# Kernel tuning notes

Hardware: AMD Instinct MI355X
Metric: run time of the kernel (lower is better)

Reference implementation:

```python
import jax, jax.numpy as jnp
import numpy as np

D_MODEL = 1024
NUM_HEADS = 16
DILATION_RATES = [2, 2, 2]
SEGMENT_SIZES = [64, 128, 256]
BATCH = 2
SEQ_LEN = 8192
N_LAYERS = len(SEGMENT_SIZES)


def setup_inputs() -> dict:
    key = jax.random.key(0)
    ks = jax.random.split(key, 5)
    d = D_MODEL
    scale = 1.0 / np.sqrt(d)
    x = jax.random.normal(ks[0], (BATCH, SEQ_LEN, d), dtype=jnp.float32)
    # Per-layer fused QKV + output projection params (stacked over layers)
    Wqkv = jax.random.normal(ks[1], (N_LAYERS, d, 3 * d), dtype=jnp.float32) * scale
    bqkv = jnp.zeros((N_LAYERS, 3 * d), dtype=jnp.float32)
    Wo = jax.random.normal(ks[2], (N_LAYERS, d, d), dtype=jnp.float32) * scale
    bo = jnp.zeros((N_LAYERS, d), dtype=jnp.float32)
    return {"x": x, "Wqkv": Wqkv, "bqkv": bqkv, "Wo": Wo, "bo": bo}


def _dilated_attention(x, Wqkv, bqkv, Wo, bo, seg, dr):
    # x: [B, S, D]. Segment, then dilate-stride within each segment.
    B, S, D = x.shape
    H = NUM_HEADS
    hd = D // H
    x4 = x.reshape(B, S // seg, seg, D)[:, :, ::dr, :]  # [B, N, s, D], s = seg//dr
    s = seg // dr
    N = S // seg
    qkv = jnp.einsum('bnsd,de->bnse', x4, Wqkv) + bqkv  # [B, N, s, 3D]
    q, k, v = jnp.split(qkv, 3, axis=-1)
    q = q.reshape(B, N, s, H, hd)
    k = k.reshape(B, N, s, H, hd)
    v = v.reshape(B, N, s, H, hd)
    # attention within each dilated segment
    scores = jnp.einsum('bnqhd,bnkhd->bnhqk', q, k) * (1.0 / np.sqrt(hd))
    attn = jax.nn.softmax(scores, axis=-1)
    o = jnp.einsum('bnhqk,bnkhd->bnqhd', attn, v).reshape(B, N, s, D)
    o = jnp.einsum('bnsd,de->bnse', o, Wo) + bo
    return o.reshape(B, N * s, D)  # [B, S/dr, D]


def reference(x, Wqkv, bqkv, Wo, bo):
    outs = []
    for i in range(N_LAYERS):
        outs.append(_dilated_attention(x, Wqkv[i], bqkv[i], Wo[i], bo[i],
                                       SEGMENT_SIZES[i], DILATION_RATES[i]))
    return jnp.stack(outs, axis=0).sum(axis=0)
```

## Files before the change

kernel.cpp:

```cpp
#include <hip/hip_runtime.h>
#include <hip/hip_bf16.h>
#include <stdint.h>

typedef unsigned short u16;
typedef short bf16x8 __attribute__((ext_vector_type(8)));
typedef u16   u16x8  __attribute__((ext_vector_type(8)));
typedef u16   u16x4  __attribute__((ext_vector_type(4)));
typedef float f32x4  __attribute__((ext_vector_type(4)));

__device__ inline u16 f2bf(float f) {
    uint32_t u = __builtin_bit_cast(uint32_t, f);
    uint32_t r = (u + 0x7FFFu + ((u >> 16) & 1u)) >> 16;
    return (u16)r;
}

__device__ inline void gload16(const void* g, void* l) {
    __builtin_amdgcn_global_load_lds((const __attribute__((address_space(1))) void*)g,
                                     (__attribute__((address_space(3))) void*)l, 16, 0, 0);
}

#define MFMA16(a, b, c) __builtin_amdgcn_mfma_f32_16x16x32_bf16((a), (b), (c), 0, 0, 0)

__global__ __launch_bounds__(256) void k_prep_xe(const float* __restrict__ x,
                                                 u16* __restrict__ xe) {
    int row = blockIdx.x;
    int b = row >> 12, tt = row & 4095;
    const float* src = x + ((size_t)b * 8192 + 2 * (size_t)tt) * 1024;
    float4 v = ((const float4*)src)[threadIdx.x];
    u16x4 o = { f2bf(v.x), f2bf(v.y), f2bf(v.z), f2bf(v.w) };
    *(u16x4*)(xe + (size_t)row * 1024 + threadIdx.x * 4) = o;
}

__global__ __launch_bounds__(256) void k_transpose_cast(
    const float* __restrict__ src, u16* __restrict__ dst,
    int srcCols, size_t srcLayerStride, int dstStride, int dstRowPer, int dstColPer) {
    int k0 = blockIdx.x * 64, e0 = blockIdx.y * 64, layer = blockIdx.z;
    const float* s = src + (size_t)layer * srcLayerStride;
    __shared__ u16 T[64][66];
    int t = threadIdx.x;
#pragma unroll
    for (int p = 0; p < 16; ++p) {
        int l = p * 256 + t;
        int kl = l >> 6, el = l & 63;
        T[kl][el] = f2bf(s[(size_t)(k0 + kl) * srcCols + e0 + el]);
    }
    __syncthreads();
    int rowBase = layer * dstRowPer + e0;
    int colBase = layer * dstColPer + k0;
#pragma unroll
    for (int p = 0; p < 16; ++p) {
        int l = p * 256 + t;
        int eo = l >> 6, ko = l & 63;
        dst[(size_t)(rowBase + eo) * dstStride + colBase + ko] = T[ko][eo];
    }
}

template <bool BF16OUT>
__global__ __launch_bounds__(256) void k_gemm_bt(
    const u16* __restrict__ A, const u16* __restrict__ B, void* __restrict__ C,
    const float* __restrict__ bias0, const float* __restrict__ bias1,
    const float* __restrict__ bias2, int K, int lda, int ldb, int ldc) {
    __shared__ __align__(16) char smem[16384];
    const int tid = threadIdx.x;
    const int lane = tid & 63, wave = tid >> 6;
    const int wr = wave >> 1, wc = wave & 1;
    const int row0 = blockIdx.x * 128, col0 = blockIdx.y * 128;
    f32x4 acc[4][4] = {};
    const int nk = K >> 5;
    const char* Abase = (const char*)(A + (size_t)row0 * lda);
    const char* Bbase = (const char*)(B + (size_t)col0 * ldb);
    char* ldsA = smem;
    char* ldsB = smem + 8192;
    const size_t lda2 = (size_t)lda * 2, ldb2 = (size_t)ldb * 2;
    const int c0 = tid;
    const int c1 = tid + 256;

    for (int ks = 0; ks < nk; ++ks) {
        const size_t kb0 = (size_t)(ks * 32) * 2;
        gload16(Abase + (size_t)(c0 >> 2) * lda2 + kb0 + (c0 & 3) * 16, ldsA + wave * 1024);
        gload16(Abase + (size_t)(c1 >> 2) * lda2 + kb0 + (c1 & 3) * 16, ldsA + 4096 + wave * 1024);
        gload16(Bbase + (size_t)(c0 >> 2) * ldb2 + kb0 + (c0 & 3) * 16, ldsB + wave * 1024);
        gload16(Bbase + (size_t)(c1 >> 2) * ldb2 + kb0 + (c1 & 3) * 16, ldsB + 4096 + wave * 1024);
        __syncthreads();
        bf16x8 af[4], bfr[4];
        const int kb = (lane >> 4) << 4;
#pragma unroll
        for (int mt = 0; mt < 4; ++mt)
            af[mt] = *(const bf16x8*)(ldsA + (wr * 64 + mt * 16 + (lane & 15)) * 64 + kb);
#pragma unroll
        for (int nt = 0; nt < 4; ++nt)
            bfr[nt] = *(const bf16x8*)(ldsB + (wc * 64 + nt * 16 + (lane & 15)) * 64 + kb);
#pragma unroll
        for (int mt = 0; mt < 4; ++mt)
#pragma unroll
            for (int nt = 0; nt < 4; ++nt)
                acc[mt][nt] = MFMA16(af[mt], bfr[nt], acc[mt][nt]);
        __syncthreads();
    }
    const int g = lane >> 4, cl = lane & 15;
#pragma unroll
    for (int nt = 0; nt < 4; ++nt) {
        int col = col0 + wc * 64 + nt * 16 + cl;
        float bs = bias0[col];
        if (bias1) bs += bias1[col];
        if (bias2) bs += bias2[col];
#pragma unroll
        for (int mt = 0; mt < 4; ++mt) {
#pragma unroll
            for (int r = 0; r < 4; ++r) {
                int row = row0 + wr * 64 + mt * 16 + g * 4 + r;
                float v = acc[mt][nt][r] + bs;
                if (BF16OUT)
                    ((u16*)C)[(size_t)row * ldc + col] = f2bf(v);
                else
                    ((float*)C)[(size_t)row * ldc + col] = v;
            }
        }
    }
}

template <int S>
__global__ __launch_bounds__(256) void k_attn(const u16* __restrict__ qkv,
                                              u16* __restrict__ ab, int layer) {
    constexpr int NCT = S / 16;
    constexpr int RPW = (S == 32) ? 1 : S / 64;
    constexpr int ACTIVE = (S == 32) ? 2 : 4;
    constexpr int KST = S / 32;
    constexpr int VSTRIDE = 2 * S;
    constexpr int VMASK = VSTRIDE / 16 - 1;

    __shared__ __align__(16) char KS[S * 128];
    __shared__ __align__(16) char VTS[64 * VSTRIDE];
    __shared__ __align__(16) char PS[S * VSTRIDE];

    const int per_b = (4096 / S) * 16;
    const int b = blockIdx.x / per_b;
    const int r0 = blockIdx.x % per_b;
    const int n = r0 >> 4, h = r0 & 15;
    const int token0 = b * 4096 + n * S;
    const int colQ = layer * 3072 + h * 64;
    const int tid = threadIdx.x, lane = tid & 63, wave = tid >> 6;

    constexpr int CHUNKS = S / 32;
#pragma unroll
    for (int c = 0; c < CHUNKS; ++c) {
        int lc = c * 256 + tid;
        int row = lc >> 3, off = (lc & 7) * 16;
        const char* base = (const char*)qkv + ((size_t)(token0 + row) * 9216 + colQ) * 2 + off;
        u16x8 kv = *(const u16x8*)(base + 1024 * 2);
        *(u16x8*)(KS + row * 128 + (off ^ ((row & 7) << 4))) = kv;
        u16x8 vv = *(const u16x8*)(base + 2048 * 2);
        int cb = off >> 1;
#pragma unroll
        for (int e = 0; e < 8; ++e) {
            int col = cb + e;
            *(u16*)(VTS + col * VSTRIDE + ((row * 2) ^ ((col & VMASK) << 4))) = vv[e];
        }
    }
    __syncthreads();

    f32x4 sacc[RPW][NCT] = {};
    if (wave < ACTIVE) {
#pragma unroll
        for (int rl = 0; rl < RPW; ++rl) {
            int rt = wave * RPW + rl;
#pragma unroll
            for (int ks2 = 0; ks2 < 2; ++ks2) {
                int qrow = token0 + rt * 16 + (lane & 15);
                int kbyte = ks2 * 64 + ((lane >> 4) << 4);
                bf16x8 aq = *(const bf16x8*)((const char*)qkv +
                              ((size_t)qrow * 9216 + colQ) * 2 + kbyte);
#pragma unroll
                for (int ct = 0; ct < NCT; ++ct) {
                    int krow = ct * 16 + (lane & 15);
                    bf16x8 bk = *(const bf16x8*)(KS + krow * 128 + (kbyte ^ ((krow & 7) << 4)));
                    sacc[rl][ct] = MFMA16(aq, bk, sacc[rl][ct]);
                }
            }
        }
#pragma unroll
        for (int rl = 0; rl < RPW; ++rl) {
            int rt = wave * RPW + rl;
#pragma unroll
            for (int r = 0; r < 4; ++r) {
                float vals[NCT];
                float m = -1e30f;
#pragma unroll
                for (int ct = 0; ct < NCT; ++ct) {
                    vals[ct] = sacc[rl][ct][r] * 0.125f;
                    m = fmaxf(m, vals[ct]);
                }
#pragma unroll
                for (int d = 1; d < 16; d <<= 1) m = fmaxf(m, __shfl_xor(m, d, 64));
                float sum = 0.f;
#pragma unroll
                for (int ct = 0; ct < NCT; ++ct) {
                    float p = exp2f((vals[ct] - m) * 1.44269504f);
                    vals[ct] = p;
                    sum += p;
                }
#pragma unroll
                for (int d = 1; d < 16; d <<= 1) sum += __shfl_xor(sum, d, 64);
                float inv = 1.0f / sum;
                int row = rt * 16 + ((lane >> 4) << 2) + r;
#pragma unroll
                for (int ct = 0; ct < NCT; ++ct) {
                    int col = ct * 16 + (lane & 15);
                    *(u16*)(PS + row * VSTRIDE + ((col * 2) ^ ((row & VMASK) << 4))) =
                        f2bf(vals[ct] * inv);
                }
            }
        }
    }
    __syncthreads();

    if (wave < ACTIVE) {
        const int colA = layer * 1024 + h * 64;
#pragma unroll
        for (int rl = 0; rl < RPW; ++rl) {
            int rt = wave * RPW + rl;
            f32x4 oacc[4] = {};
#pragma unroll
            for (int ks2 = 0; ks2 < KST; ++ks2) {
                int kbyte = ks2 * 64 + ((lane >> 4) << 4);
                int prow = rt * 16 + (lane & 15);
                bf16x8 ap = *(const bf16x8*)(PS + prow * VSTRIDE + (kbyte ^ ((prow & VMASK) << 4)));
#pragma unroll
                for (int ct = 0; ct < 4; ++ct) {
                    int vcol = ct * 16 + (lane & 15);
                    bf16x8 bv = *(const bf16x8*)(VTS + vcol * VSTRIDE + (kbyte ^ ((vcol & VMASK) << 4)));
                    oacc[ct] = MFMA16(ap, bv, oacc[ct]);
                }
            }
#pragma unroll
            for (int ct = 0; ct < 4; ++ct) {
#pragma unroll
                for (int r = 0; r < 4; ++r) {
                    int row = token0 + rt * 16 + ((lane >> 4) << 2) + r;
                    int col = colA + ct * 16 + (lane & 15);
                    ab[(size_t)row * 3072 + col] = f2bf(oacc[ct][r]);
                }
            }
        }
    }
}

extern "C" void kernel_launch(void* const* d_in, const int* in_sizes, int n_in,
                              void* d_out, int out_size, void* d_ws, size_t ws_size,
                              hipStream_t stream) {
    const float* x    = (const float*)d_in[0];
    const float* Wqkv = (const float*)d_in[1];
    const float* bqkv = (const float*)d_in[2];
    const float* Wo   = (const float*)d_in[3];
    const float* bo   = (const float*)d_in[4];

    char* ws = (char*)d_ws;
    u16* XE    = (u16*)(ws);
    u16* WQKVT = (u16*)(ws + 16777216);
    u16* WOT   = (u16*)(ws + 35651584);
    u16* QKVB  = (u16*)(ws + 41943040);
    u16* ABUF  = (u16*)(ws + 192937984);

    k_prep_xe<<<8192, 256, 0, stream>>>(x, XE);
    k_transpose_cast<<<dim3(16, 48, 3), 256, 0, stream>>>(
        Wqkv, WQKVT, 3072, (size_t)1024 * 3072, 1024, 3072, 0);
    k_transpose_cast<<<dim3(16, 16, 3), 256, 0, stream>>>(
        Wo, WOT, 1024, (size_t)1024 * 1024, 3072, 0, 1024);

    k_gemm_bt<true><<<dim3(64, 72), 256, 0, stream>>>(
        XE, WQKVT, QKVB, bqkv, nullptr, nullptr, 1024, 1024, 1024, 9216);

    k_attn<32><<<4096, 256, 0, stream>>>(QKVB, ABUF, 0);
    k_attn<64><<<2048, 256, 0, stream>>>(QKVB, ABUF, 1);
    k_attn<128><<<1024, 256, 0, stream>>>(QKVB, ABUF, 2);

    k_gemm_bt<false><<<dim3(64, 8), 256, 0, stream>>>(
        ABUF, WOT, d_out, bo, bo + 1024, bo + 2048, 3072, 3072, 3072, 1024);
}
```

Measured before the change: 366.5 us.

## Replace QKV GEMM with 256x256 tile, 4-stage pipelined, swizzled kernel

Adds a new 512-thread GEMM kernel with 256x256 output tiles, a 4-deep LDS ring filled by direct global-to-LDS loads, XOR-swizzled LDS layout, and explicit barriers with scheduling priority to overlap loads with MFMA work. Workgroups are remapped in groups of eight for L2 locality. It replaces the 128x128 GEMM for the QKV projection (8192x9216x1024). The aim is more data reuse per tile and hidden memory latency. The cost is 128KB of LDS per block, which limits occupancy, and a more fragile pipeline schedule.

```diff
diff --git a/kernel.cpp b/kernel.cpp
--- a/kernel.cpp
+++ b/kernel.cpp
@@ -17,6 +17,12 @@
 __device__ inline void gload16(const void* g, void* l) {
     __builtin_amdgcn_global_load_lds((const __attribute__((address_space(1))) void*)g,
                                      (__attribute__((address_space(3))) void*)l, 16, 0, 0);
+}
+
+__device__ inline void pin_barrier() {
+    __builtin_amdgcn_sched_barrier(0);
+    __builtin_amdgcn_s_barrier();
+    __builtin_amdgcn_sched_barrier(0);
 }
 
 #define MFMA16(a, b, c) __builtin_amdgcn_mfma_f32_16x16x32_bf16((a), (b), (c), 0, 0, 0)
@@ -53,6 +59,114 @@
         int eo = l >> 6, ko = l & 63;
         dst[(size_t)(rowBase + eo) * dstStride + colBase + ko] = T[ko][eo];
     }
+}
+
+__global__ __launch_bounds__(512, 2) void k_gemm256(
+    const u16* __restrict__ A, const u16* __restrict__ B, u16* __restrict__ C,
+    const float* __restrict__ bias, int K, int lda, int ldb, int ldc,
+    int gxmask, int gxshift) {
+    __shared__ __align__(16) char smem[131072];
+    const int tid = threadIdx.x;
+    const int lane = tid & 63, wave = tid >> 6;
+    const int wr = wave >> 2, wc = wave & 3;
+
+    const int nwg = gridDim.x;
+    const int bid = blockIdx.x;
+    const int cpx = nwg >> 3;
+    const int swz = (bid & 7) * cpx + (bid >> 3);
+    const int bx = swz & gxmask;
+    const int by = swz >> gxshift;
+    const int row0 = bx << 8, col0 = by << 8;
+
+#define SA(q) (smem + (q) * 32768)
+#define SB(q) (smem + (q) * 32768 + 16384)
+
+    const int c0 = tid, c1 = tid + 512;
+    const int rA0 = ((c0 >> 6) << 4) + ((c0 >> 2) & 15);
+    const int rA1 = ((c1 >> 6) << 4) + ((c1 >> 2) & 15);
+    const int cb0 = ((c0 & 3) * 16) ^ (((c0 >> 5) & 1) << 5);
+    const int cb1 = ((c1 & 3) * 16) ^ (((c1 >> 5) & 1) << 5);
+    const size_t lda2 = (size_t)lda * 2, ldb2 = (size_t)ldb * 2;
+    const char* pA0 = (const char*)A + (size_t)(row0 + rA0) * lda2 + cb0;
+    const char* pA1 = (const char*)A + (size_t)(row0 + rA1) * lda2 + cb1;
+    const char* pB0 = (const char*)B + (size_t)(col0 + rA0) * ldb2 + cb0;
+    const char* pB1 = (const char*)B + (size_t)(col0 + rA1) * ldb2 + cb1;
+    const int ldsOff0 = wave * 1024, ldsOff1 = 8192 + wave * 1024;
+
+#define STAGE_A(q, kof) do { gload16(pA0 + (kof), SA(q) + ldsOff0); \
+                             gload16(pA1 + (kof), SA(q) + ldsOff1); } while (0)
+#define STAGE_B(q, kof) do { gload16(pB0 + (kof), SB(q) + ldsOff0); \
+                             gload16(pB1 + (kof), SB(q) + ldsOff1); } while (0)
+
+    const int lane_off = (lane & 15) * 64 + (((lane >> 4) << 4) ^ (((lane >> 3) & 1) << 5));
+
+    f32x4 acc[8][4] = {};
+    const int nt = K >> 5;
+
+    STAGE_A(0, 0);   STAGE_B(0, 0);
+    STAGE_A(1, 64);  STAGE_B(1, 64);
+    STAGE_A(2, 128); STAGE_B(2, 128);
+    __builtin_amdgcn_sched_barrier(0);
+    asm volatile("s_waitcnt vmcnt(8)" ::: "memory");
+    pin_barrier();
+
+    for (int t = 0; t < nt; ++t) {
+        const int q = t & 3, q3 = (t + 3) & 3;
+        const int ts = (t + 3 < nt) ? (t + 3) : (nt - 1);
+        const size_t kof = (size_t)ts * 64;
+        const char* aRd = SA(q) + wr * 8192 + lane_off;
+        const char* bRd = SB(q) + wc * 4096 + lane_off;
+
+        bf16x8 af[4], bg[4];
+#pragma unroll
+        for (int i = 0; i < 4; ++i) af[i] = *(const bf16x8*)(aRd + i * 1024);
+#pragma unroll
+        for (int i = 0; i < 4; ++i) bg[i] = *(const bf16x8*)(bRd + i * 1024);
+        STAGE_A(q3, kof);
+        pin_barrier();
+        __builtin_amdgcn_s_setprio(1);
+#pragma unroll
+        for (int m = 0; m < 4; ++m)
+#pragma unroll
+            for (int n = 0; n < 4; ++n)
+                acc[m][n] = MFMA16(af[m], bg[n], acc[m][n]);
+        __builtin_amdgcn_s_setprio(0);
+        pin_barrier();
+
+#pragma unroll
+        for (int i = 0; i < 4; ++i) af[i] = *(const bf16x8*)(aRd + (4 + i) * 1024);
+        STAGE_B(q3, kof);
+        __builtin_amdgcn_sched_barrier(0);
+        asm volatile("s_waitcnt vmcnt(8)" ::: "memory");
+        pin_barrier();
+        __builtin_amdgcn_s_setprio(1);
+#pragma unroll
+        for (int m = 0; m < 4; ++m)
+#pragma unroll
+            for (int n = 0; n < 4; ++n)
+                acc[4 + m][n] = MFMA16(af[m], bg[n], acc[4 + m][n]);
+        __builtin_amdgcn_s_setprio(0);
+        pin_barrier();
+    }
+
+    const int g4 = (lane >> 4) << 2, cl = lane & 15;
+#pragma unroll
+    for (int n = 0; n < 4; ++n) {
+        int col = col0 + wc * 64 + n * 16 + cl;
+        float bs = bias[col];
+#pragma unroll
+        for (int m = 0; m < 8; ++m) {
+#pragma unroll
+            for (int r = 0; r < 4; ++r) {
+                int row = row0 + wr * 128 + m * 16 + g4 + r;
+                C[(size_t)row * ldc + col] = f2bf(acc[m][n][r] + bs);
+            }
+        }
+    }
+#undef SA
+#undef SB
+#undef STAGE_A
+#undef STAGE_B
 }
 
 template <bool BF16OUT>
@@ -267,8 +381,8 @@
     k_transpose_cast<<<dim3(16, 16, 3), 256, 0, stream>>>(
         Wo, WOT, 1024, (size_t)1024 * 1024, 3072, 0, 1024);
 
-    k_gemm_bt<true><<<dim3(64, 72), 256, 0, stream>>>(
-        XE, WQKVT, QKVB, bqkv, nullptr, nullptr, 1024, 1024, 1024, 9216);
+    k_gemm256<<<dim3(1152), 512, 0, stream>>>(
+        XE, WQKVT, QKVB, bqkv, 1024, 1024, 1024, 9216, 31, 5);
 
     k_attn<32><<<4096, 256, 0, stream>>>(QKVB, ABUF, 0);
     k_attn<64><<<2048, 256, 0, stream>>>(QKVB, ABUF, 1);
```

New measurement: 360.5 us. No clear change (-1.6%).

## Replace GEMM with 256-row tiles, register-staged double-buffered LDS pipeline and swizzles

Applied to the files above, without the earlier changes.

Replaces the simple single-buffered 128x128 GEMM with a 512-thread kernel that uses 256xBN tiles. Global loads go into registers and are written to ping-pong LDS buffers while MFMAs run on the other buffer, with explicit waitcnt and sched barriers. It also adds an XOR swizzle on the LDS layout, a grid swizzle for L2 locality, and an epilogue that stages output through LDS so stores are coalesced and 16 bytes wide. The aim is to hide global-load latency and raise MFMA utilisation for the QKV and output projections. In exchange, the 128KB of static LDS limits occupancy to one block per CU, and the hand-written waitcnt counts are fragile.

```diff
diff --git a/kernel.cpp b/kernel.cpp
--- a/kernel.cpp
+++ b/kernel.cpp
@@ -14,9 +14,10 @@
     return (u16)r;
 }
 
-__device__ inline void gload16(const void* g, void* l) {
-    __builtin_amdgcn_global_load_lds((const __attribute__((address_space(1))) void*)g,
-                                     (__attribute__((address_space(3))) void*)l, 16, 0, 0);
+__device__ inline void pin_barrier() {
+    __builtin_amdgcn_sched_barrier(0);
+    __builtin_amdgcn_s_barrier();
+    __builtin_amdgcn_sched_barrier(0);
 }
 
 #define MFMA16(a, b, c) __builtin_amdgcn_mfma_f32_16x16x32_bf16((a), (b), (c), 0, 0, 0)
@@ -55,66 +56,154 @@
     }
 }
 
-template <bool BF16OUT>
-__global__ __launch_bounds__(256) void k_gemm_bt(
+template <int BN, bool BF16OUT>
+__global__ __launch_bounds__(512, 2) void k_gemm_rs(
     const u16* __restrict__ A, const u16* __restrict__ B, void* __restrict__ C,
     const float* __restrict__ bias0, const float* __restrict__ bias1,
-    const float* __restrict__ bias2, int K, int lda, int ldb, int ldc) {
-    __shared__ __align__(16) char smem[16384];
-    const int tid = threadIdx.x;
-    const int lane = tid & 63, wave = tid >> 6;
-    const int wr = wave >> 1, wc = wave & 1;
-    const int row0 = blockIdx.x * 128, col0 = blockIdx.y * 128;
-    f32x4 acc[4][4] = {};
-    const int nk = K >> 5;
-    const char* Abase = (const char*)(A + (size_t)row0 * lda);
-    const char* Bbase = (const char*)(B + (size_t)col0 * ldb);
-    char* ldsA = smem;
-    char* ldsB = smem + 8192;
+    const float* __restrict__ bias2, int K, int lda, int ldb, int ldc,
+    int gxmask, int gxshift) {
+    constexpr int WN = BN / 64;
+    constexpr int WM = 8 / WN;
+    constexpr int MF = 256 / (WM * 16);
+    constexpr int NF = 4;
+    constexpr int NCA = 2;
+    constexpr int NCB = (BN * 4) / 512;
+    constexpr int NL = NCA + NCB;
+    constexpr int SBUF = 16384 + BN * 64;
+
+    __shared__ __align__(16) char smem[131072];
+    const int tid = threadIdx.x, lane = tid & 63, wave = tid >> 6;
+    const int wr = wave / WN, wc = wave % WN;
+
+    const int nwg = gridDim.x, bid = blockIdx.x;
+    const int cpx = nwg >> 3;
+    const int swz = (bid & 7) * cpx + (bid >> 3);
+    const int bx = swz & gxmask, by = swz >> gxshift;
+    const int row0 = bx << 8;
+    const int col0 = by * BN;
+
     const size_t lda2 = (size_t)lda * 2, ldb2 = (size_t)ldb * 2;
-    const int c0 = tid;
-    const int c1 = tid + 256;
-
-    for (int ks = 0; ks < nk; ++ks) {
-        const size_t kb0 = (size_t)(ks * 32) * 2;
-        gload16(Abase + (size_t)(c0 >> 2) * lda2 + kb0 + (c0 & 3) * 16, ldsA + wave * 1024);
-        gload16(Abase + (size_t)(c1 >> 2) * lda2 + kb0 + (c1 & 3) * 16, ldsA + 4096 + wave * 1024);
-        gload16(Bbase + (size_t)(c0 >> 2) * ldb2 + kb0 + (c0 & 3) * 16, ldsB + wave * 1024);
-        gload16(Bbase + (size_t)(c1 >> 2) * ldb2 + kb0 + (c1 & 3) * 16, ldsB + 4096 + wave * 1024);
-        __syncthreads();
-        bf16x8 af[4], bfr[4];
-        const int kb = (lane >> 4) << 4;
-#pragma unroll
-        for (int mt = 0; mt < 4; ++mt)
-            af[mt] = *(const bf16x8*)(ldsA + (wr * 64 + mt * 16 + (lane & 15)) * 64 + kb);
-#pragma unroll
-        for (int nt = 0; nt < 4; ++nt)
-            bfr[nt] = *(const bf16x8*)(ldsB + (wc * 64 + nt * 16 + (lane & 15)) * 64 + kb);
-#pragma unroll
-        for (int mt = 0; mt < 4; ++mt)
-#pragma unroll
-            for (int nt = 0; nt < 4; ++nt)
-                acc[mt][nt] = MFMA16(af[mt], bfr[nt], acc[mt][nt]);
-        __syncthreads();
-    }
-    const int g = lane >> 4, cl = lane & 15;
-#pragma unroll
-    for (int nt = 0; nt < 4; ++nt) {
-        int col = col0 + wc * 64 + nt * 16 + cl;
-        float bs = bias0[col];
-        if (bias1) bs += bias1[col];
-        if (bias2) bs += bias2[col];
-#pragma unroll
-        for (int mt = 0; mt < 4; ++mt) {
-#pragma unroll
-            for (int r = 0; r < 4; ++r) {
-                int row = row0 + wr * 64 + mt * 16 + g * 4 + r;
-                float v = acc[mt][nt][r] + bs;
-                if (BF16OUT)
-                    ((u16*)C)[(size_t)row * ldc + col] = f2bf(v);
-                else
-                    ((float*)C)[(size_t)row * ldc + col] = v;
-            }
+    const char* gA[NCA]; int wA[NCA];
+    const char* gB[NCB]; int wB[NCB];
+#pragma unroll
+    for (int i = 0; i < NCA; ++i) {
+        int c = tid + i * 512, row = c >> 2, cg = c & 3;
+        gA[i] = (const char*)A + (size_t)(row0 + row) * lda2 + cg * 16;
+        wA[i] = row * 64 + ((cg * 16) ^ (((row >> 3) & 1) << 5));
+    }
+#pragma unroll
+    for (int i = 0; i < NCB; ++i) {
+        int c = tid + i * 512, row = c >> 2, cg = c & 3;
+        gB[i] = (const char*)B + (size_t)(col0 + row) * ldb2 + cg * 16;
+        wB[i] = 16384 + row * 64 + ((cg * 16) ^ (((row >> 3) & 1) << 5));
+    }
+
+    const int lane_off = (lane & 15) * 64 +
+                         (((lane >> 4) << 4) ^ (((lane >> 3) & 1) << 5));
+
+    f32x4 acc[MF][NF] = {};
+    const int nt = K >> 5;
+    u16x8 uE[NL], uO[NL];
+
+    auto LOADSET = [&](u16x8* u, int ts) {
+#pragma unroll
+        for (int i = 0; i < NCA; ++i)
+            u[i] = *(const u16x8*)(gA[i] + (size_t)ts * 64);
+#pragma unroll
+        for (int i = 0; i < NCB; ++i)
+            u[NCA + i] = *(const u16x8*)(gB[i] + (size_t)ts * 64);
+    };
+    auto WRITESET = [&](const u16x8* u, char* buf) {
+#pragma unroll
+        for (int i = 0; i < NCA; ++i) *(u16x8*)(buf + wA[i]) = u[i];
+#pragma unroll
+        for (int i = 0; i < NCB; ++i) *(u16x8*)(buf + wB[i]) = u[NCA + i];
+    };
+    auto WAIT_VM_NL = [&] {
+        if constexpr (NL == 4) asm volatile("s_waitcnt vmcnt(4)" ::: "memory");
+        else                   asm volatile("s_waitcnt vmcnt(3)" ::: "memory");
+    };
+    auto WAIT_LGKM_NL = [&] {
+        if constexpr (NL == 4) asm volatile("s_waitcnt lgkmcnt(4)" ::: "memory");
+        else                   asm volatile("s_waitcnt lgkmcnt(3)" ::: "memory");
+    };
+    auto TBODY = [&](const char* bufR, const u16x8* uW, char* bufW,
+                     u16x8* uL, int tload) {
+        const char* aRd = bufR + wr * (MF * 1024) + lane_off;
+        const char* bRd = bufR + 16384 + wc * (NF * 1024) + lane_off;
+        bf16x8 af[MF], bg[NF];
+#pragma unroll
+        for (int i = 0; i < MF; ++i) af[i] = *(const bf16x8*)(aRd + i * 1024);
+#pragma unroll
+        for (int i = 0; i < NF; ++i) bg[i] = *(const bf16x8*)(bRd + i * 1024);
+        LOADSET(uL, tload);
+        WAIT_VM_NL();
+        WRITESET(uW, bufW);
+        WAIT_LGKM_NL();
+        __builtin_amdgcn_sched_barrier(0);
+        __builtin_amdgcn_s_setprio(1);
+#pragma unroll
+        for (int m = 0; m < MF; ++m)
+#pragma unroll
+            for (int n = 0; n < NF; ++n)
+                acc[m][n] = MFMA16(af[m], bg[n], acc[m][n]);
+        __builtin_amdgcn_s_setprio(0);
+        asm volatile("s_waitcnt lgkmcnt(0)" ::: "memory");
+        pin_barrier();
+    };
+
+    LOADSET(uE, 0);
+    LOADSET(uO, 1);
+    WAIT_VM_NL();
+    WRITESET(uE, smem);
+    asm volatile("s_waitcnt lgkmcnt(0)" ::: "memory");
+    pin_barrier();
+
+    char* buf0 = smem;
+    char* buf1 = smem + SBUF;
+    for (int t = 0; t < nt; t += 2) {
+        int l2 = (t + 2 < nt) ? t + 2 : nt - 1;
+        int l3 = (t + 3 < nt) ? t + 3 : nt - 1;
+        TBODY(buf0, uO, buf1, uE, l2);
+        TBODY(buf1, uE, buf0, uO, l3);
+    }
+
+    {
+        char* cst = smem;
+        const int g4 = (lane >> 4) << 2, cl = lane & 15;
+#pragma unroll
+        for (int n = 0; n < NF; ++n) {
+            int col = wc * (NF * 16) + n * 16 + cl;
+            float bs = bias0[col0 + col];
+            if (bias1) bs += bias1[col0 + col];
+            if (bias2) bs += bias2[col0 + col];
+#pragma unroll
+            for (int m = 0; m < MF; ++m) {
+#pragma unroll
+                for (int r = 0; r < 4; ++r) {
+                    int row = wr * (MF * 16) + m * 16 + g4 + r;
+                    float v = acc[m][n][r] + bs;
+                    if (BF16OUT) {
+                        int scol = col ^ (((row >> 2) & 3) << 3);
+                        *(u16*)(cst + row * 512 + scol * 2) = f2bf(v);
+                    } else {
+                        int scol = col ^ (((row >> 2) & 3) << 2);
+                        *(float*)(cst + row * 512 + scol * 4) = v;
+                    }
+                }
+            }
+        }
+        asm volatile("s_waitcnt lgkmcnt(0)" ::: "memory");
+        pin_barrier();
+        const int esz = BF16OUT ? 2 : 4;
+#pragma unroll
+        for (int it = 0; it < 16; ++it) {
+            int id = it * 512 + tid;
+            int row = id >> 5, c16 = id & 31;
+            int sc16 = c16 ^ ((row >> 2) & 3);
+            u16x8 v = *(const u16x8*)(cst + row * 512 + sc16 * 16);
+            char* dst = (char*)C + ((size_t)(row0 + row) * ldc + col0) * esz + c16 * 16;
+            *(u16x8*)dst = v;
         }
     }
 }
@@ -267,13 +356,13 @@
     k_transpose_cast<<<dim3(16, 16, 3), 256, 0, stream>>>(
         Wo, WOT, 1024, (size_t)1024 * 1024, 3072, 0, 1024);
 
-    k_gemm_bt<true><<<dim3(64, 72), 256, 0, stream>>>(
-        XE, WQKVT, QKVB, bqkv, nullptr, nullptr, 1024, 1024, 1024, 9216);
+    k_gemm_rs<256, true><<<dim3(1152), 512, 0, stream>>>(
+        XE, WQKVT, QKVB, bqkv, nullptr, nullptr, 1024, 1024, 1024, 9216, 31, 5);
 
     k_attn<32><<<4096, 256, 0, stream>>>(QKVB, ABUF, 0);
     k_attn<64><<<2048, 256, 0, stream>>>(QKVB, ABUF, 1);
     k_attn<128><<<1024, 256, 0, stream>>>(QKVB, ABUF, 2);
 
-    k_gemm_bt<false><<<dim3(64, 8), 256, 0, stream>>>(
-        ABUF, WOT, d_out, bo, bo + 1024, bo + 2048, 3072, 3072, 3072, 1024);
-}
+    k_gemm_rs<128, false><<<dim3(256), 512, 0, stream>>>(
+        ABUF, WOT, d_out, bo, bo + 1024, bo + 2048, 3072, 3072, 3072, 1024, 31, 5);
+}
```

Measured after the change: 327.9 us. 10.5% less time.
